# Optimization experiments

Hardware: AMD Instinct MI355X
Metric: run time of the kernel (lower is better)

## Reference

```python
import jax, jax.numpy as jnp
import numpy as np

N_BINS = 15
TEMP = 1.0


def setup_inputs() -> dict:
    key = jax.random.key(0)
    k1, k2 = jax.random.split(key)
    N, C = 1000000, 100
    probs = jax.random.uniform(k1, (N, C), dtype=jnp.float32)
    labels = jax.random.randint(k2, (N,), 0, C, dtype=jnp.int64)
    return {"probs": probs, "labels": labels}


def reference(probs, labels):
    # apply_log=True, temp=1.0: p = softmax(log(probs)/temp)
    p = jax.nn.softmax(jnp.log(probs) / TEMP, axis=-1)  # [N, C]
    confidences = jnp.max(p, axis=1)                     # [N]
    predictions = jnp.argmax(p, axis=1)                  # [N]
    accuracies = (predictions == labels).astype(p.dtype)

    one_hot = jax.nn.one_hot(labels, p.shape[-1], dtype=p.dtype)
    bri = jnp.mean(jnp.sum((p - one_hot) ** 2, axis=1))  # mean squared L2 norm

    # bins are (i/n_bins, (i+1)/n_bins]; conf > 0 always (softmax max >= 1/C)
    bin_idx = jnp.clip(jnp.ceil(confidences * N_BINS).astype(jnp.int32) - 1, 0, N_BINS - 1)

    ones = jnp.ones_like(confidences)
    counts = jax.ops.segment_sum(ones, bin_idx, num_segments=N_BINS)
    sum_conf = jax.ops.segment_sum(confidences, bin_idx, num_segments=N_BINS)
    sum_acc = jax.ops.segment_sum(accuracies, bin_idx, num_segments=N_BINS)

    nonempty = counts > 0
    safe = jnp.maximum(counts, 1.0)
    gap = jnp.where(nonempty, jnp.abs(sum_conf / safe - sum_acc / safe), 0.0)  # [n_bins]
    prop = counts / confidences.shape[0]

    ece = jnp.sum(gap * prop)
    max_err = jnp.max(gap)  # matches torch init of 0.0 for all-empty case
    return jnp.stack([ece, max_err, bri])
```

## Files before the change

### kernel.cpp

```cpp
#include <hip/hip_runtime.h>

#define NBINS 15

__global__ __launch_bounds__(256) void ece_rows(const float* __restrict__ probs,
                                                const int* __restrict__ labels,
                                                int N, int C,
                                                double* __restrict__ g_bri,
                                                float* __restrict__ g_cnt,
                                                float* __restrict__ g_conf,
                                                float* __restrict__ g_acc) {
    __shared__ float s_hist[3][64][NBINS];
    __shared__ float s_bri;
    const int tid = threadIdx.x;
    for (int i = tid; i < 3 * 64 * NBINS; i += 256)
        ((float*)s_hist)[i] = 0.f;
    if (tid == 0) s_bri = 0.f;
    __syncthreads();

    const int l   = tid & 3;
    const int grp = tid >> 2;
    float tbri = 0.f;

    const int r0      = blockIdx.x * 64 + grp;
    const int rstride = gridDim.x * 64;

    for (int r = r0; r < N; r += rstride) {
        const float4* row4 = (const float4*)(probs + (size_t)r * 100);

        float4 v[6];
        #pragma unroll
        for (int j = 0; j < 6; j++) v[j] = row4[j * 4 + l];

        float sum = 0.f, sq = 0.f, vmax = -1.f;
        int imax = 0;
        #pragma unroll
        for (int j = 0; j < 6; j++) {
            float4 u = v[j];
            int c = (j * 4 + l) * 4;
            sum += (u.x + u.y) + (u.z + u.w);
            sq = fmaf(u.x, u.x, sq);
            sq = fmaf(u.y, u.y, sq);
            sq = fmaf(u.z, u.z, sq);
            sq = fmaf(u.w, u.w, sq);
            if (u.x > vmax) { vmax = u.x; imax = c; }
            if (u.y > vmax) { vmax = u.y; imax = c + 1; }
            if (u.z > vmax) { vmax = u.z; imax = c + 2; }
            if (u.w > vmax) { vmax = u.w; imax = c + 3; }
        }
        if (l == 0) {
            float4 u = row4[24];
            sum += (u.x + u.y) + (u.z + u.w);
            sq = fmaf(u.x, u.x, sq);
            sq = fmaf(u.y, u.y, sq);
            sq = fmaf(u.z, u.z, sq);
            sq = fmaf(u.w, u.w, sq);
            if (u.x > vmax) { vmax = u.x; imax = 96; }
            if (u.y > vmax) { vmax = u.y; imax = 97; }
            if (u.z > vmax) { vmax = u.z; imax = 98; }
            if (u.w > vmax) { vmax = u.w; imax = 99; }
        }

        #pragma unroll
        for (int off = 1; off <= 2; off <<= 1) {
            sum += __shfl_xor(sum, off);
            sq  += __shfl_xor(sq,  off);
            float ov = __shfl_xor(vmax, off);
            int   oi = __shfl_xor(imax, off);
            if (ov > vmax || (ov == vmax && oi < imax)) { vmax = ov; imax = oi; }
        }

        if (l == 0) {
            const int label = labels[r];
            const float pl = ((const float*)row4)[label];
            const float inv = 1.f / sum;
            const float conf = vmax * inv;
            const float acc = (imax == label) ? 1.f : 0.f;
            tbri += sq * inv * inv - 2.f * (pl * inv) + 1.f;

            int bin = (int)ceilf(conf * (float)NBINS) - 1;
            bin = bin < 0 ? 0 : (bin > NBINS - 1 ? NBINS - 1 : bin);
            s_hist[0][grp][bin] += 1.f;
            s_hist[1][grp][bin] += conf;
            s_hist[2][grp][bin] += acc;
        }
    }

    #pragma unroll
    for (int off = 32; off > 0; off >>= 1)
        tbri += __shfl_down(tbri, off);
    if ((tid & 63) == 0) atomicAdd(&s_bri, tbri);
    __syncthreads();

    if (tid < 3 * NBINS) {
        const int a = tid / NBINS, b = tid % NBINS;
        float acc = 0.f;
        #pragma unroll
        for (int g = 0; g < 64; g++) acc += s_hist[a][g][b];
        float* dst = (a == 0) ? g_cnt : (a == 1) ? g_conf : g_acc;
        atomicAdd(&dst[b], acc);
    }
    if (tid == 0) atomicAdd(g_bri, (double)s_bri);
}

__global__ void ece_final(const double* __restrict__ g_bri,
                          const float* __restrict__ g_cnt,
                          const float* __restrict__ g_conf,
                          const float* __restrict__ g_acc,
                          float* __restrict__ out, float invN) {
    if (threadIdx.x == 0 && blockIdx.x == 0) {
        float ece = 0.f, mx = 0.f;
        for (int b = 0; b < NBINS; b++) {
            float c = g_cnt[b];
            float gap = 0.f;
            if (c > 0.f) gap = fabsf(g_conf[b] / c - g_acc[b] / c);
            ece += gap * (c * invN);
            if (gap > mx) mx = gap;
        }
        out[0] = ece;
        out[1] = mx;
        out[2] = (float)(g_bri[0] * (double)invN);
    }
}

extern "C" void kernel_launch(void* const* d_in, const int* in_sizes, int n_in,
                              void* d_out, int out_size, void* d_ws, size_t ws_size,
                              hipStream_t stream) {
    const float* probs  = (const float*)d_in[0];
    const int*   labels = (const int*)d_in[1];
    const int N = in_sizes[1];

    double* g_bri  = (double*)d_ws;
    float*  g_cnt  = (float*)((char*)d_ws + sizeof(double));
    float*  g_conf = g_cnt + NBINS;
    float*  g_acc  = g_conf + NBINS;

    hipMemsetAsync(d_ws, 0, sizeof(double) + 3 * NBINS * sizeof(float), stream);

    const int blocks = 2048;
    hipLaunchKernelGGL(ece_rows, dim3(blocks), dim3(256), 0, stream,
                       probs, labels, N, 100, g_bri, g_cnt, g_conf, g_acc);
    hipLaunchKernelGGL(ece_final, dim3(1), dim3(64), 0, stream,
                       g_bri, g_cnt, g_conf, g_acc, (float*)d_out, 1.f / (float)N);
}
```

Before: 546.1 us.

## Stage row tiles through LDS with fully coalesced float4 loads

Each block now loads a 64-row tile (6400 floats) into padded shared memory using contiguous, fully coalesced float4 loads per wavefront, then computes per-row statistics from LDS. Previously each 4-lane group read its own row with strided float4 accesses. The label-indexed lookup also comes from LDS instead of a second global read. It adds two block barriers per tile and more LDS use, which may reduce occupancy, and it changes the grid size to 3125 blocks.

```diff
diff --git a/kernel.cpp b/kernel.cpp
--- a/kernel.cpp
+++ b/kernel.cpp
@@ -1,101 +1,131 @@
 #include <hip/hip_runtime.h>
 
 #define NBINS 15
+#define RPI   64
+#define PADF4 26
 
 __global__ __launch_bounds__(256) void ece_rows(const float* __restrict__ probs,
                                                 const int* __restrict__ labels,
-                                                int N, int C,
+                                                int N,
                                                 double* __restrict__ g_bri,
                                                 float* __restrict__ g_cnt,
                                                 float* __restrict__ g_conf,
                                                 float* __restrict__ g_acc) {
-    __shared__ float s_hist[3][64][NBINS];
-    __shared__ float s_bri;
+    __shared__ float4 s_buf[RPI * PADF4];
+    __shared__ float  s_hist[3][RPI][NBINS];
+    __shared__ float  s_bri;
     const int tid = threadIdx.x;
-    for (int i = tid; i < 3 * 64 * NBINS; i += 256)
+    for (int i = tid; i < 3 * RPI * NBINS; i += 256)
         ((float*)s_hist)[i] = 0.f;
     if (tid == 0) s_bri = 0.f;
-    __syncthreads();
 
-    const int l   = tid & 3;
-    const int grp = tid >> 2;
+    const int lane = tid & 63;
+    const int w    = tid >> 6;
+    const int l    = tid & 3;
+    const int grp  = tid >> 2;
     float tbri = 0.f;
 
-    const int r0      = blockIdx.x * 64 + grp;
-    const int rstride = gridDim.x * 64;
+    const float4* g4 = (const float4*)probs;
+    const int itersTotal = (N + RPI - 1) / RPI;
 
-    for (int r = r0; r < N; r += rstride) {
-        const float4* row4 = (const float4*)(probs + (size_t)r * 100);
+    for (int it = blockIdx.x; it < itersTotal; it += gridDim.x) {
+        const int rbase = it * RPI;
+        const int rows_here = min(RPI, N - rbase);
 
-        float4 v[6];
-        #pragma unroll
-        for (int j = 0; j < 6; j++) v[j] = row4[j * 4 + l];
+        if (rows_here == RPI) {
+            const size_t gbase = (size_t)(rbase + 16 * w) * 25;
+            #pragma unroll
+            for (int t = 0; t < 6; t++) {
+                int k = t * 64 + lane;
+                float4 v = g4[gbase + k];
+                int lr = k / 25, lp = k - lr * 25;
+                s_buf[(16 * w + lr) * PADF4 + lp] = v;
+            }
+            if (lane < 16) {
+                int k = 384 + lane;
+                float4 v = g4[gbase + k];
+                int lr = k / 25, lp = k - lr * 25;
+                s_buf[(16 * w + lr) * PADF4 + lp] = v;
+            }
+        } else {
+            for (int k = tid; k < rows_here * 25; k += 256) {
+                float4 v = g4[(size_t)rbase * 25 + k];
+                int lr = k / 25, lp = k - lr * 25;
+                s_buf[lr * PADF4 + lp] = v;
+            }
+        }
+        __syncthreads();
 
-        float sum = 0.f, sq = 0.f, vmax = -1.f;
-        int imax = 0;
-        #pragma unroll
-        for (int j = 0; j < 6; j++) {
-            float4 u = v[j];
-            int c = (j * 4 + l) * 4;
-            sum += (u.x + u.y) + (u.z + u.w);
-            sq = fmaf(u.x, u.x, sq);
-            sq = fmaf(u.y, u.y, sq);
-            sq = fmaf(u.z, u.z, sq);
-            sq = fmaf(u.w, u.w, sq);
-            if (u.x > vmax) { vmax = u.x; imax = c; }
-            if (u.y > vmax) { vmax = u.y; imax = c + 1; }
-            if (u.z > vmax) { vmax = u.z; imax = c + 2; }
-            if (u.w > vmax) { vmax = u.w; imax = c + 3; }
+        const int r = rbase + grp;
+        if (r < N) {
+            const float4* rowb = &s_buf[grp * PADF4];
+            float sum = 0.f, sq = 0.f, vmax = -1.f;
+            int imax = 0;
+            float4 v[6];
+            #pragma unroll
+            for (int j = 0; j < 6; j++) v[j] = rowb[4 * j + l];
+            #pragma unroll
+            for (int j = 0; j < 6; j++) {
+                float4 u = v[j];
+                int c = (4 * j + l) * 4;
+                sum += (u.x + u.y) + (u.z + u.w);
+                sq = fmaf(u.x, u.x, sq);
+                sq = fmaf(u.y, u.y, sq);
+                sq = fmaf(u.z, u.z, sq);
+                sq = fmaf(u.w, u.w, sq);
+                if (u.x > vmax) { vmax = u.x; imax = c; }
+                if (u.y > vmax) { vmax = u.y; imax = c + 1; }
+                if (u.z > vmax) { vmax = u.z; imax = c + 2; }
+                if (u.w > vmax) { vmax = u.w; imax = c + 3; }
+            }
+            if (l == 0) {
+                float4 u = rowb[24];
+                sum += (u.x + u.y) + (u.z + u.w);
+                sq = fmaf(u.x, u.x, sq);
+                sq = fmaf(u.y, u.y, sq);
+                sq = fmaf(u.z, u.z, sq);
+                sq = fmaf(u.w, u.w, sq);
+                if (u.x > vmax) { vmax = u.x; imax = 96; }
+                if (u.y > vmax) { vmax = u.y; imax = 97; }
+                if (u.z > vmax) { vmax = u.z; imax = 98; }
+                if (u.w > vmax) { vmax = u.w; imax = 99; }
+            }
+            #pragma unroll
+            for (int off = 1; off <= 2; off <<= 1) {
+                sum += __shfl_xor(sum, off);
+                sq  += __shfl_xor(sq,  off);
+                float ov = __shfl_xor(vmax, off);
+                int   oi = __shfl_xor(imax, off);
+                if (ov > vmax || (ov == vmax && oi < imax)) { vmax = ov; imax = oi; }
+            }
+            if (l == 0) {
+                const int label = labels[r];
+                const float pl = ((const float*)rowb)[label];
+                const float inv = 1.f / sum;
+                const float conf = vmax * inv;
+                const float acc = (imax == label) ? 1.f : 0.f;
+                tbri += sq * inv * inv - 2.f * (pl * inv) + 1.f;
+                int bin = (int)ceilf(conf * (float)NBINS) - 1;
+                bin = bin < 0 ? 0 : (bin > NBINS - 1 ? NBINS - 1 : bin);
+                s_hist[0][grp][bin] += 1.f;
+                s_hist[1][grp][bin] += conf;
+                s_hist[2][grp][bin] += acc;
+            }
         }
-        if (l == 0) {
-            float4 u = row4[24];
-            sum += (u.x + u.y) + (u.z + u.w);
-            sq = fmaf(u.x, u.x, sq);
-            sq = fmaf(u.y, u.y, sq);
-            sq = fmaf(u.z, u.z, sq);
-            sq = fmaf(u.w, u.w, sq);
-            if (u.x > vmax) { vmax = u.x; imax = 96; }
-            if (u.y > vmax) { vmax = u.y; imax = 97; }
-            if (u.z > vmax) { vmax = u.z; imax = 98; }
-            if (u.w > vmax) { vmax = u.w; imax = 99; }
-        }
-
-        #pragma unroll
-        for (int off = 1; off <= 2; off <<= 1) {
-            sum += __shfl_xor(sum, off);
-            sq  += __shfl_xor(sq,  off);
-            float ov = __shfl_xor(vmax, off);
-            int   oi = __shfl_xor(imax, off);
-            if (ov > vmax || (ov == vmax && oi < imax)) { vmax = ov; imax = oi; }
-        }
-
-        if (l == 0) {
-            const int label = labels[r];
-            const float pl = ((const float*)row4)[label];
-            const float inv = 1.f / sum;
-            const float conf = vmax * inv;
-            const float acc = (imax == label) ? 1.f : 0.f;
-            tbri += sq * inv * inv - 2.f * (pl * inv) + 1.f;
-
-            int bin = (int)ceilf(conf * (float)NBINS) - 1;
-            bin = bin < 0 ? 0 : (bin > NBINS - 1 ? NBINS - 1 : bin);
-            s_hist[0][grp][bin] += 1.f;
-            s_hist[1][grp][bin] += conf;
-            s_hist[2][grp][bin] += acc;
-        }
+        __syncthreads();
     }
 
     #pragma unroll
     for (int off = 32; off > 0; off >>= 1)
         tbri += __shfl_down(tbri, off);
-    if ((tid & 63) == 0) atomicAdd(&s_bri, tbri);
+    if (lane == 0) atomicAdd(&s_bri, tbri);
     __syncthreads();
 
     if (tid < 3 * NBINS) {
         const int a = tid / NBINS, b = tid % NBINS;
         float acc = 0.f;
         #pragma unroll
-        for (int g = 0; g < 64; g++) acc += s_hist[a][g][b];
+        for (int g = 0; g < RPI; g++) acc += s_hist[a][g][b];
         float* dst = (a == 0) ? g_cnt : (a == 1) ? g_conf : g_acc;
         atomicAdd(&dst[b], acc);
     }
@@ -136,9 +166,10 @@
 
     hipMemsetAsync(d_ws, 0, sizeof(double) + 3 * NBINS * sizeof(float), stream);
 
-    const int blocks = 2048;
+    const int itersTotal = (N + RPI - 1) / RPI;
+    const int blocks = itersTotal < 3125 ? itersTotal : 3125;
     hipLaunchKernelGGL(ece_rows, dim3(blocks), dim3(256), 0, stream,
-                       probs, labels, N, 100, g_bri, g_cnt, g_conf, g_acc);
+                       probs, labels, N, g_bri, g_cnt, g_conf, g_acc);
     hipLaunchKernelGGL(ece_final, dim3(1), dim3(64), 0, stream,
                        g_bri, g_cnt, g_conf, g_acc, (float*)d_out, 1.f / (float)N);
 }
```

New measurement: 560.0 us. 1.03x slower.
